# Performance work log

Measured on AMD Instinct MI355X. Metric: run time of the kernel, lower is better.

## Reference

```python
import jax, jax.numpy as jnp
import numpy as np

_MIN_BLOCK_KV = 32


def setup_inputs() -> dict:
    key = jax.random.key(0)
    k0, k1, k2, k3 = jax.random.split(key, 4)
    B, H, HKV, D, T, S = 32, 32, 8, 128, 2048, 8
    pool = B * T
    q = jax.random.normal(k0, (B, H, D), dtype=jnp.float32)
    k_buffer = jax.random.normal(k1, (pool, HKV, D), dtype=jnp.float32)
    v_buffer = jax.random.normal(k2, (pool, HKV, D), dtype=jnp.float32)
    # uniform contexts: request b owns tokens [b*T, (b+1)*T) of the pool, in permuted (paged) order
    kv_indptr = (jnp.arange(B + 1, dtype=jnp.int32) * T)
    kv_indices = jax.random.permutation(k3, pool).astype(jnp.int32)
    num_kv_splits = jnp.full((B,), S, dtype=jnp.int32)
    return {"q": q, "k_buffer": k_buffer, "v_buffer": v_buffer,
            "kv_indptr": kv_indptr, "kv_indices": kv_indices,
            "num_kv_splits": num_kv_splits}


def reference(q, k_buffer, v_buffer, kv_indptr, kv_indices, num_kv_splits):
    # Paged KV-cache decode attention, stage 1 (split-KV partial softmax).
    B, H, D = q.shape
    HKV = k_buffer.shape[1]
    Lv = v_buffer.shape[-1]
    G = H // HKV                       # GQA group size
    sm_scale = 1.0 / (D ** 0.5)        # Model default (sm_scale=None)
    logit_cap = 0.0                    # Model default -> capping disabled

    seq_lens = kv_indptr[1:] - kv_indptr[:-1]          # [B]
    T = kv_indices.shape[0] // B                       # max context len (uniform setup)
    S = int(jnp.max(num_kv_splits))                    # max_kv_splits (eager, as in torch code)

    pos = jnp.arange(T, dtype=jnp.int32)               # [T]
    valid = pos[None, :] < seq_lens[:, None]           # [B,T]
    # gather KV pool locations per (batch, position); clamp OOB positions
    gidx = kv_indptr[:-1, None] + jnp.minimum(pos[None, :], seq_lens[:, None] - 1)
    kv_loc = kv_indices[gidx]                          # [B,T]
    k_g = k_buffer[kv_loc]                             # [B,T,HKV,D]
    v_g = v_buffer[kv_loc]                             # [B,T,HKV,Lv]

    qr = q.reshape(B, HKV, G, D)
    qk = jnp.einsum('bkgd,btkd->bkgt', qr, k_g) * sm_scale   # [B,HKV,G,T]
    if logit_cap > 0:
        qk = logit_cap * jnp.tanh(qk / logit_cap)

    # split assignment: kv_len_per_split = cdiv(cdiv(seq_len, splits), MIN) * MIN
    cdiv = lambda a, b: (a + b - 1) // b
    kv_len_per_split = cdiv(cdiv(seq_lens, num_kv_splits), _MIN_BLOCK_KV) * _MIN_BLOCK_KV  # [B]
    split_id = pos[None, :] // kv_len_per_split[:, None]      # [B,T]
    split_mask = (split_id[:, None, :] == jnp.arange(S, dtype=jnp.int32)[None, :, None]) \
                 & valid[:, None, :]                          # [B,S,T]

    neg_inf = jnp.float32(-jnp.inf)
    masked = jnp.where(split_mask[:, None, None, :, :], qk[:, :, :, None, :], neg_inf)  # [B,HKV,G,S,T]
    m = jnp.max(masked, axis=-1)                               # [B,HKV,G,S]
    m_safe = jnp.where(jnp.isfinite(m), m, 0.0)                # guard empty splits
    p = jnp.exp(masked - m_safe[..., None])                    # [B,HKV,G,S,T]
    p = jnp.where(split_mask[:, None, None, :, :], p, 0.0)
    e_sum = jnp.sum(p, axis=-1)                                # [B,HKV,G,S]
    acc = jnp.einsum('bkgst,btkv->bkgsv', p, v_g)              # [B,HKV,G,S,Lv]

    att_out = (acc / e_sum[..., None]).reshape(B, H, S, Lv)
    att_lse = (m + jnp.log(e_sum)).reshape(B, H, S)
    return att_out, att_lse
```

## Files before the change

kernel.cpp:

```cpp
#include <hip/hip_runtime.h>
#include <math.h>


namespace {
constexpr int kB = 32;
constexpr int kH = 32;
constexpr int kHKV = 8;
constexpr int kD = 128;
constexpr int kG = kH / kHKV;
constexpr int kS = 8;
constexpr int kMinBlockKV = 32;
constexpr int kHB = 4;
constexpr int kTT = 8;
constexpr int kChunk = 512;
}

__device__ __forceinline__ void gload16_nt(const float* g, float* l) {
    __builtin_amdgcn_global_load_lds(
        (const __attribute__((address_space(1))) void*)g,
        (__attribute__((address_space(3))) void*)l,
        16, 0, 18);
}

__global__ __launch_bounds__(512, 2) void decode_split_kernel(
    const float* __restrict__ q,
    const float* __restrict__ k_buffer,
    const float* __restrict__ v_buffer,
    const int* __restrict__ kv_indptr,
    const int* __restrict__ kv_indices,
    const int* __restrict__ num_kv_splits,
    float* __restrict__ att_out,
    float* __restrict__ att_lse)
{
    const int bid = blockIdx.x;
    const int hh  = bid & 1;
    const int s   = (bid >> 1) & (kS - 1);
    const int b   = bid >> 4;
    const int kh0 = hh * kHB;

    const int tid  = threadIdx.x;
    const int wave = tid >> 6;
    const int lane = tid & 63;
    const int tg   = lane >> 4;
    const int li   = lane & 15;
    const int hkv_l = wave >> 1;
    const int sub   = wave & 1;

    const int ptr0    = kv_indptr[b];
    const int seq_len = kv_indptr[b + 1] - ptr0;
    const int splits  = num_kv_splits[b];
    const int per     = (seq_len + splits - 1) / splits;
    const int lps     = ((per + kMinBlockKV - 1) / kMinBlockKV) * kMinBlockKV;
    const int t0 = s * lps;
    const int t1 = min(t0 + lps, seq_len);

    const float sm_scale = 0.08838834764831845f;

    __shared__ float stage[2][kTT][2][kHB * kD];

    float4 q0[kG], q1[kG];
    const float* qb = q + ((size_t)b * kH + (size_t)(kh0 + hkv_l) * kG) * kD;
    #pragma unroll
    for (int g = 0; g < kG; ++g) {
        float4 a = *(const float4*)(qb + (size_t)g * kD + li * 4);
        float4 c = *(const float4*)(qb + (size_t)g * kD + 64 + li * 4);
        q0[g] = make_float4(a.x * sm_scale, a.y * sm_scale, a.z * sm_scale, a.w * sm_scale);
        q1[g] = make_float4(c.x * sm_scale, c.y * sm_scale, c.z * sm_scale, c.w * sm_scale);
    }

    float  l[kG] = {0.f, 0.f, 0.f, 0.f};
    float4 a0[kG], a1[kG];
    #pragma unroll
    for (int g = 0; g < kG; ++g) {
        a0[g] = make_float4(0.f, 0.f, 0.f, 0.f);
        a1[g] = make_float4(0.f, 0.f, 0.f, 0.f);
    }

    for (int chunk = t0; chunk < t1; chunk += kChunk) {
        const int nt    = min(kChunk, t1 - chunk);
        const int ntile = (nt + kTT - 1) / kTT;

        int my_loc = kv_indices[ptr0 + min(chunk + lane * kTT + wave, t1 - 1)];
        asm volatile("s_waitcnt vmcnt(0) lgkmcnt(0)" ::: "memory");

#define ISSUE(T)                                                             \
        {                                                                    \
            const int _loc = __shfl(my_loc, (T));                            \
            float* _dk = &stage[(T) & 1][wave][0][0];                        \
            float* _dv = &stage[(T) & 1][wave][1][0];                        \
            const float* _kb = k_buffer + ((size_t)_loc * kHKV + kh0) * kD + lane * 4; \
            const float* _vb = v_buffer + ((size_t)_loc * kHKV + kh0) * kD + lane * 4; \
            gload16_nt(_kb,       _dk);                                      \
            gload16_nt(_kb + 256, _dk + 256);                                \
            gload16_nt(_vb,       _dv);                                      \
            gload16_nt(_vb + 256, _dv + 256);                                \
        }

        if (ntile > 0) ISSUE(0)
        if (ntile > 1) ISSUE(1)

        for (int t = 0; t < ntile; ++t) {
            if (t + 1 < ntile) { asm volatile("s_waitcnt vmcnt(4)" ::: "memory"); }
            else               { asm volatile("s_waitcnt vmcnt(0)" ::: "memory"); }
            __builtin_amdgcn_s_barrier();
            __builtin_amdgcn_sched_barrier(0);

            const float* kp = &stage[t & 1][sub * 4 + tg][0][hkv_l * kD];
            const float* vp = &stage[t & 1][sub * 4 + tg][1][hkv_l * kD];
            float4 ck0 = *(const float4*)(kp + li * 4);
            float4 ck1 = *(const float4*)(kp + 64 + li * 4);
            float4 cv0 = *(const float4*)(vp + li * 4);
            float4 cv1 = *(const float4*)(vp + 64 + li * 4);

            asm volatile("s_waitcnt lgkmcnt(0)" ::: "memory");
            __builtin_amdgcn_sched_barrier(0);
            __builtin_amdgcn_s_barrier();

            if (t + 2 < ntile) ISSUE(t + 2)

            float dot[kG];
            #pragma unroll
            for (int g = 0; g < kG; ++g) {
                float d = q0[g].x * ck0.x;
                d = fmaf(q0[g].y, ck0.y, d);
                d = fmaf(q0[g].z, ck0.z, d);
                d = fmaf(q0[g].w, ck0.w, d);
                d = fmaf(q1[g].x, ck1.x, d);
                d = fmaf(q1[g].y, ck1.y, d);
                d = fmaf(q1[g].z, ck1.z, d);
                d = fmaf(q1[g].w, ck1.w, d);
                dot[g] = d;
            }
            #pragma unroll
            for (int m = 1; m <= 8; m <<= 1) {
                #pragma unroll
                for (int g = 0; g < kG; ++g)
                    dot[g] += __shfl_xor(dot[g], m);
            }

            const bool valid = (t * kTT + sub * 4 + tg) < nt;
            #pragma unroll
            for (int g = 0; g < kG; ++g) {
                const float p = valid ? __expf(dot[g]) : 0.f;
                l[g] += p;
                a0[g].x = fmaf(p, cv0.x, a0[g].x);
                a0[g].y = fmaf(p, cv0.y, a0[g].y);
                a0[g].z = fmaf(p, cv0.z, a0[g].z);
                a0[g].w = fmaf(p, cv0.w, a0[g].w);
                a1[g].x = fmaf(p, cv1.x, a1[g].x);
                a1[g].y = fmaf(p, cv1.y, a1[g].y);
                a1[g].z = fmaf(p, cv1.z, a1[g].z);
                a1[g].w = fmaf(p, cv1.w, a1[g].w);
            }
        }
#undef ISSUE
    }

    #pragma unroll
    for (int m = 16; m <= 32; m <<= 1) {
        #pragma unroll
        for (int g = 0; g < kG; ++g) {
            a0[g].x += __shfl_xor(a0[g].x, m);
            a0[g].y += __shfl_xor(a0[g].y, m);
            a0[g].z += __shfl_xor(a0[g].z, m);
            a0[g].w += __shfl_xor(a0[g].w, m);
            a1[g].x += __shfl_xor(a1[g].x, m);
            a1[g].y += __shfl_xor(a1[g].y, m);
            a1[g].z += __shfl_xor(a1[g].z, m);
            a1[g].w += __shfl_xor(a1[g].w, m);
            l[g] += __shfl_xor(l[g], m);
        }
    }

    __syncthreads();
    float* comb  = &stage[0][0][0][0];
    float* combl = comb + 4096;
    if (tg == 0) {
        const int base = (hkv_l * 2 + sub) * kG;
        #pragma unroll
        for (int g = 0; g < kG; ++g) {
            *(float4*)&comb[(base + g) * kD + li * 4]      = a0[g];
            *(float4*)&comb[(base + g) * kD + 64 + li * 4] = a1[g];
        }
        if (li == 0) {
            #pragma unroll
            for (int g = 0; g < kG; ++g) combl[base + g] = l[g];
        }
    }
    __syncthreads();

    const int ohkv = tid >> 7;
    const int og   = (tid >> 5) & 3;
    const int od   = (tid & 31) * 4;
    const int i0 = (ohkv * 2 + 0) * kG + og;
    const int i1 = (ohkv * 2 + 1) * kG + og;
    float4 x0 = *(float4*)&comb[i0 * kD + od];
    float4 x1 = *(float4*)&comb[i1 * kD + od];
    const float ls  = combl[i0] + combl[i1];
    const float inv = 1.0f / ls;
    float4 o;
    o.x = (x0.x + x1.x) * inv;
    o.y = (x0.y + x1.y) * inv;
    o.z = (x0.z + x1.z) * inv;
    o.w = (x0.w + x1.w) * inv;
    const size_t hidx = (size_t)b * kH + (size_t)(kh0 + ohkv) * kG + og;
    *(float4*)(att_out + (hidx * kS + s) * kD + od) = o;
    if (od == 0)
        att_lse[hidx * kS + s] = logf(ls);
}

extern "C" void kernel_launch(void* const* d_in, const int* in_sizes, int n_in,
                              void* d_out, int out_size, void* d_ws, size_t ws_size,
                              hipStream_t stream) {
    const float* q             = (const float*)d_in[0];
    const float* k_buffer      = (const float*)d_in[1];
    const float* v_buffer      = (const float*)d_in[2];
    const int*   kv_indptr     = (const int*)d_in[3];
    const int*   kv_indices    = (const int*)d_in[4];
    const int*   num_kv_splits = (const int*)d_in[5];

    float* att_out = (float*)d_out;
    float* att_lse = att_out + (size_t)kB * kH * kS * kD;

    dim3 grid(kB * kS * 2);
    decode_split_kernel<<<grid, 512, 0, stream>>>(
        q, k_buffer, v_buffer, kv_indptr, kv_indices, num_kv_splits,
        att_out, att_lse);
}
```

Baseline: 486.6 us.

## Merge KV-head halves into one 1024-thread block loading full token rows

Each block now covers all 8 KV heads for one (batch, split) pair instead of half of them, so the grid is halved and blocks grow to 1024 threads with 128 KB of dynamic LDS. Each staged token row is a contiguous 4 KB K or V slice, loaded by separate K and V waves, instead of two 2 KB halves fetched by different blocks. This aims at better DRAM and gather locality and at reading kv_indices once per token rather than twice. The cost is one large block per CU, fewer blocks to hide latency, and a one-time host attribute call for the larger LDS size.

```diff
diff --git a/kernel.cpp b/kernel.cpp
--- a/kernel.cpp
+++ b/kernel.cpp
@@ -10,8 +10,9 @@
 constexpr int kG = kH / kHKV;
 constexpr int kS = 8;
 constexpr int kMinBlockKV = 32;
-constexpr int kHB = 4;
 constexpr int kTT = 8;
+constexpr int kRowF = kHKV * kD;
+constexpr int kSlotF = kTT * 2 * kRowF;
 constexpr int kChunk = 512;
 }
 
@@ -22,7 +23,7 @@
         16, 0, 18);
 }
 
-__global__ __launch_bounds__(512, 2) void decode_split_kernel(
+__global__ __launch_bounds__(1024, 1) void decode_split_kernel(
     const float* __restrict__ q,
     const float* __restrict__ k_buffer,
     const float* __restrict__ v_buffer,
@@ -33,18 +34,18 @@
     float* __restrict__ att_lse)
 {
     const int bid = blockIdx.x;
-    const int hh  = bid & 1;
-    const int s   = (bid >> 1) & (kS - 1);
-    const int b   = bid >> 4;
-    const int kh0 = hh * kHB;
+    const int s   = bid & (kS - 1);
+    const int b   = bid >> 3;
 
     const int tid  = threadIdx.x;
     const int wave = tid >> 6;
     const int lane = tid & 63;
     const int tg   = lane >> 4;
     const int li   = lane & 15;
-    const int hkv_l = wave >> 1;
-    const int sub   = wave & 1;
+    const int tok   = wave & 7;
+    const int kvsel = wave >> 3;
+    const int h     = wave & 7;
+    const int thal  = wave >> 3;
 
     const int ptr0    = kv_indptr[b];
     const int seq_len = kv_indptr[b + 1] - ptr0;
@@ -56,10 +57,10 @@
 
     const float sm_scale = 0.08838834764831845f;
 
-    __shared__ float stage[2][kTT][2][kHB * kD];
+    extern __shared__ float stage[];
 
     float4 q0[kG], q1[kG];
-    const float* qb = q + ((size_t)b * kH + (size_t)(kh0 + hkv_l) * kG) * kD;
+    const float* qb = q + ((size_t)b * kH + (size_t)h * kG) * kD;
     #pragma unroll
     for (int g = 0; g < kG; ++g) {
         float4 a = *(const float4*)(qb + (size_t)g * kD + li * 4);
@@ -80,20 +81,20 @@
         const int nt    = min(kChunk, t1 - chunk);
         const int ntile = (nt + kTT - 1) / kTT;
 
-        int my_loc = kv_indices[ptr0 + min(chunk + lane * kTT + wave, t1 - 1)];
+        int my_loc = kv_indices[ptr0 + min(chunk + lane * kTT + tok, t1 - 1)];
         asm volatile("s_waitcnt vmcnt(0) lgkmcnt(0)" ::: "memory");
 
 #define ISSUE(T)                                                             \
         {                                                                    \
             const int _loc = __shfl(my_loc, (T));                            \
-            float* _dk = &stage[(T) & 1][wave][0][0];                        \
-            float* _dv = &stage[(T) & 1][wave][1][0];                        \
-            const float* _kb = k_buffer + ((size_t)_loc * kHKV + kh0) * kD + lane * 4; \
-            const float* _vb = v_buffer + ((size_t)_loc * kHKV + kh0) * kD + lane * 4; \
-            gload16_nt(_kb,       _dk);                                      \
-            gload16_nt(_kb + 256, _dk + 256);                                \
-            gload16_nt(_vb,       _dv);                                      \
-            gload16_nt(_vb + 256, _dv + 256);                                \
+            float* _d = stage + ((T) & 1) * kSlotF + tok * (2 * kRowF)       \
+                              + kvsel * kRowF;                               \
+            const float* _src = (kvsel ? v_buffer : k_buffer)                \
+                              + (size_t)_loc * kRowF + lane * 4;             \
+            gload16_nt(_src,       _d);                                      \
+            gload16_nt(_src + 256, _d + 256);                                \
+            gload16_nt(_src + 512, _d + 512);                                \
+            gload16_nt(_src + 768, _d + 768);                                \
         }
 
         if (ntile > 0) ISSUE(0)
@@ -105,8 +106,9 @@
             __builtin_amdgcn_s_barrier();
             __builtin_amdgcn_sched_barrier(0);
 
-            const float* kp = &stage[t & 1][sub * 4 + tg][0][hkv_l * kD];
-            const float* vp = &stage[t & 1][sub * 4 + tg][1][hkv_l * kD];
+            const int tc = thal * 4 + tg;
+            const float* kp = stage + (t & 1) * kSlotF + tc * (2 * kRowF) + h * kD;
+            const float* vp = kp + kRowF;
             float4 ck0 = *(const float4*)(kp + li * 4);
             float4 ck1 = *(const float4*)(kp + 64 + li * 4);
             float4 cv0 = *(const float4*)(vp + li * 4);
@@ -138,7 +140,7 @@
                     dot[g] += __shfl_xor(dot[g], m);
             }
 
-            const bool valid = (t * kTT + sub * 4 + tg) < nt;
+            const bool valid = (t * kTT + tc) < nt;
             #pragma unroll
             for (int g = 0; g < kG; ++g) {
                 const float p = valid ? __expf(dot[g]) : 0.f;
@@ -173,27 +175,26 @@
     }
 
     __syncthreads();
-    float* comb  = &stage[0][0][0][0];
-    float* combl = comb + 4096;
+    float* comb  = stage;
+    float* combl = stage + 16 * kG * kD;
     if (tg == 0) {
-        const int base = (hkv_l * 2 + sub) * kG;
         #pragma unroll
         for (int g = 0; g < kG; ++g) {
-            *(float4*)&comb[(base + g) * kD + li * 4]      = a0[g];
-            *(float4*)&comb[(base + g) * kD + 64 + li * 4] = a1[g];
+            *(float4*)&comb[(wave * kG + g) * kD + li * 4]      = a0[g];
+            *(float4*)&comb[(wave * kG + g) * kD + 64 + li * 4] = a1[g];
         }
         if (li == 0) {
             #pragma unroll
-            for (int g = 0; g < kG; ++g) combl[base + g] = l[g];
+            for (int g = 0; g < kG; ++g) combl[wave * kG + g] = l[g];
         }
     }
     __syncthreads();
 
-    const int ohkv = tid >> 7;
-    const int og   = (tid >> 5) & 3;
-    const int od   = (tid & 31) * 4;
-    const int i0 = (ohkv * 2 + 0) * kG + og;
-    const int i1 = (ohkv * 2 + 1) * kG + og;
+    const int oh = tid >> 7;
+    const int og = (tid >> 5) & 3;
+    const int od = (tid & 31) * 4;
+    const int i0 = oh * kG + og;
+    const int i1 = (oh + 8) * kG + og;
     float4 x0 = *(float4*)&comb[i0 * kD + od];
     float4 x1 = *(float4*)&comb[i1 * kD + od];
     const float ls  = combl[i0] + combl[i1];
@@ -203,9 +204,9 @@
     o.y = (x0.y + x1.y) * inv;
     o.z = (x0.z + x1.z) * inv;
     o.w = (x0.w + x1.w) * inv;
-    const size_t hidx = (size_t)b * kH + (size_t)(kh0 + ohkv) * kG + og;
+    const size_t hidx = (size_t)b * kH + (size_t)oh * kG + og;
     *(float4*)(att_out + (hidx * kS + s) * kD + od) = o;
-    if (od == 0)
+    if ((tid & 31) == 0)
         att_lse[hidx * kS + s] = logf(ls);
 }
 
@@ -222,8 +223,17 @@
     float* att_out = (float*)d_out;
     float* att_lse = att_out + (size_t)kB * kH * kS * kD;
 
-    dim3 grid(kB * kS * 2);
-    decode_split_kernel<<<grid, 512, 0, stream>>>(
+    constexpr int kLDSBytes = 2 * kSlotF * sizeof(float);
+    static bool attr_set = false;
+    if (!attr_set) {
+        (void)hipFuncSetAttribute(
+            reinterpret_cast<const void*>(decode_split_kernel),
+            hipFuncAttributeMaxDynamicSharedMemorySize, kLDSBytes);
+        attr_set = true;
+    }
+
+    dim3 grid(kB * kS);
+    decode_split_kernel<<<grid, 1024, kLDSBytes, stream>>>(
         q, k_buffer, v_buffer, kv_indptr, kv_indices, num_kv_splits,
         att_out, att_lse);
 }
```

New measurement: 485.3 us. No clear change (-0.3%).
